# Kernel optimization log

Hardware: AMD Instinct MI355X
Metric: run time of the kernel (lower is better)

## Reference

```python
import jax, jax.numpy as jnp
import numpy as np
from jax import lax

G = 8  # number of RBF grid points (FastKAN default style)
GRID = jnp.linspace(-2.0, 2.0, G)
DENOM = 4.0 / (G - 1)  # grid spacing used as gaussian width


def _fastkan_conv(x, ln_w, ln_b, Wb, bb, Ws):
    # x: [B, C, H, W]; 3x3 conv, stride 1, pad 1 via patch unfold + FastKAN linear
    B, C, H, W = x.shape
    p = lax.conv_general_dilated_patches(x, (3, 3), (1, 1), ((1, 1), (1, 1)))  # [B, C*9, H, W]
    p = p.transpose(0, 2, 3, 1).reshape(B * H * W, C * 9)  # [N, in]
    # LayerNorm over patch features (FastKAN normalizes before the RBF basis)
    mu = p.mean(-1, keepdims=True)
    var = p.var(-1, keepdims=True)
    pn = (p - mu) / jnp.sqrt(var + 1e-5) * ln_w + ln_b
    # Gaussian RBF basis: [N, in, G]
    rbf = jnp.exp(-jnp.square((pn[:, :, None] - GRID) / DENOM))
    spline = rbf.reshape(B * H * W, -1) @ Ws.T          # [N, out]
    base = jax.nn.silu(p) @ Wb.T + bb                    # [N, out]
    out = spline + base
    return out.reshape(B, H, W, -1).transpose(0, 3, 1, 2)  # [B, out, H, W]


def _bn_relu_pool(h, gamma, beta):
    # BatchNorm2d in training mode (batch stats), ReLU, MaxPool2d(2,2)
    mu = h.mean((0, 2, 3), keepdims=True)
    var = h.var((0, 2, 3), keepdims=True)
    h = (h - mu) / jnp.sqrt(var + 1e-5) * gamma[None, :, None, None] + beta[None, :, None, None]
    h = jax.nn.relu(h)
    return lax.reduce_window(h, -jnp.inf, lax.max, (1, 1, 2, 2), (1, 1, 2, 2), 'VALID')


def setup_inputs() -> dict:
    key = jax.random.key(0)
    ks = jax.random.split(key, 16)
    B, Cin, H, W = 32, 16, 64, 64
    dims = [(Cin * 9, 64), (64 * 9, 128), (128 * 9, 256)]
    inp = {"x": jax.random.normal(ks[0], (B, Cin, H, W), jnp.float32)}
    for i, (fin, fout) in enumerate(dims, 1):
        inp[f"ln_w{i}"] = jnp.ones((fin,), jnp.float32)
        inp[f"ln_b{i}"] = jnp.zeros((fin,), jnp.float32)
        inp[f"Wb{i}"] = jax.random.normal(ks[3 * i], (fout, fin), jnp.float32) * 0.05
        inp[f"bb{i}"] = jnp.zeros((fout,), jnp.float32)
        inp[f"Ws{i}"] = jax.random.normal(ks[3 * i + 1], (fout, fin * G), jnp.float32) * 0.05
        inp[f"g{i}"] = jnp.ones((fout,), jnp.float32)
        inp[f"be{i}"] = jnp.zeros((fout,), jnp.float32)
    return inp


def reference(x, ln_w1, ln_b1, Wb1, bb1, Ws1, g1, be1,
              ln_w2, ln_b2, Wb2, bb2, Ws2, g2, be2,
              ln_w3, ln_b3, Wb3, bb3, Ws3, g3, be3):
    h = _bn_relu_pool(_fastkan_conv(x, ln_w1, ln_b1, Wb1, bb1, Ws1), g1, be1)
    h = _bn_relu_pool(_fastkan_conv(h, ln_w2, ln_b2, Wb2, bb2, Ws2), g2, be2)
    h = _bn_relu_pool(_fastkan_conv(h, ln_w3, ln_b3, Wb3, bb3, Ws3), g3, be3)
    return h.reshape(h.shape[0], -1)  # flatten: [B, 256*8*8]
```

## Files before the change

kernel.cpp:

```cpp
#include <hip/hip_runtime.h>

typedef _Float16 half_t;
typedef __attribute__((ext_vector_type(8))) _Float16 half8;
typedef __attribute__((ext_vector_type(4))) float floatx4;


#define RBF_SCALE 2.1019644f

template<int C, int H, int W>
__global__ __launch_bounds__(256)
void ln_prep(const float* __restrict__ x,
             const float* __restrict__ lnw, const float* __restrict__ lnb,
             half_t* __restrict__ pn, half_t* __restrict__ sp)
{
    const int HW = H * W, IN = C * 9;
    const int NL = (IN + 63) / 64;
    const int wv = threadIdx.x >> 6, lane = threadIdx.x & 63;
    const int pix = blockIdx.x * 4 + wv;
    const int b = pix / HW, hw = pix % HW, h = hw / W, w = hw % W;
    const float* xb = x + (long)b * C * HW;

    float v[NL];
    float s = 0.f, s2 = 0.f;
    #pragma unroll
    for (int t = 0; t < NL; ++t) {
        int i = t * 64 + lane;
        float val = 0.f;
        if (i < IN) {
            int ch = i / 9, r = i - ch * 9;
            int y = h + r / 3 - 1, xx = w + r % 3 - 1;
            if (y >= 0 && y < H && xx >= 0 && xx < W)
                val = xb[ch * HW + y * W + xx];
        }
        v[t] = val; s += val; s2 += val * val;
    }
    #pragma unroll
    for (int off = 32; off > 0; off >>= 1) {
        s  += __shfl_down(s,  off, 64);
        s2 += __shfl_down(s2, off, 64);
    }
    s = __shfl(s, 0, 64); s2 = __shfl(s2, 0, 64);
    float mean = s / IN;
    float istd = rsqrtf(s2 / IN - mean * mean + 1e-5f);

    #pragma unroll
    for (int t = 0; t < NL; ++t) {
        int i = t * 64 + lane;
        if (i < IN) {
            float val = v[t];
            float pnv = (val - mean) * istd * lnw[i] + lnb[i];
            pn[(long)pix * IN + i] = (half_t)(pnv * RBF_SCALE);
            sp[(long)pix * IN + i] = (half_t)(val / (1.f + __expf(-val)));
        }
    }
}

template<int IN, int OUT, int KPAD>
__global__ __launch_bounds__(256)
void conv_w(const float* __restrict__ Ws, const float* __restrict__ Wb,
            half_t* __restrict__ Wt)
{
    int idx = blockIdx.x * 256 + threadIdx.x;
    if (idx >= OUT * KPAD) return;
    int o = idx / KPAD, k = idx - o * KPAD;
    float v = 0.f;
    if (k < IN * 9) {
        int j = k / IN, i = k - j * IN;
        v = (j < 8) ? Ws[(long)o * IN * 8 + i * 8 + j] : Wb[(long)o * IN + i];
    }
    Wt[idx] = (half_t)v;
}

template<int IN, int OUT, int HW, int NB, int SPLIT>
__global__ __launch_bounds__(256)
void kan_gemm(const half_t* __restrict__ pn, const half_t* __restrict__ sp,
              const half_t* __restrict__ Wt, float* __restrict__ out)
{
    const int K = IN * 9, KPAD = (K + 63) & ~63, KIT = KPAD / 64;

    __shared__ half_t As[64 * 64];
    __shared__ half_t Bs[NB * 64 * 64];

    const int tid = threadIdx.x;
    const int row = tid >> 2, q = tid & 3;
    const int pix = blockIdx.x * 64 + row;
    const half_t* pnrow = pn + (long)pix * IN;
    const half_t* sprow = sp + (long)pix * IN;
    const int yoff = blockIdx.y * NB * 64;
    const half_t* wbase = Wt + (long)(yoff + row) * KPAD + q * 16;

    const int wv = tid >> 6, lane = tid & 63;
    const int lr = lane & 15, lq = lane >> 4;
    const int u0 = (2 * q) ^ (row & 7);
    const int u1 = (2 * q + 1) ^ (row & 7);

    floatx4 acc[NB][4] = {};

    const int it0 = (blockIdx.z * KIT) / SPLIT;
    const int it1 = ((blockIdx.z + 1) * KIT) / SPLIT;

    for (int it = it0; it < it1; ++it) {
        const int k0 = it * 64;
        __syncthreads();

        #pragma unroll
        for (int nb = 0; nb < NB; ++nb) {
            const uint4* src = (const uint4*)(wbase + (long)nb * 64 * KPAD + k0);
            int r2 = nb * 64 + row;
            *(uint4*)&Bs[r2 * 64 + u0 * 8] = src[0];
            *(uint4*)&Bs[r2 * 64 + u1 * 8] = src[1];
        }

        {
            int cs = k0 + q * 16;
            int j = cs / IN;
            half8 a0, a1;
            if (j < 8) {
                int i0 = cs - j * IN;
                float gj = RBF_SCALE * (-2.f + j * (4.f / 7.f));
                half8 p0 = *(const half8*)(pnrow + i0);
                half8 p1 = *(const half8*)(pnrow + i0 + 8);
                #pragma unroll
                for (int kk = 0; kk < 8; ++kk) {
                    float v0 = (float)p0[kk] - gj;
                    a0[kk] = (half_t)__builtin_amdgcn_exp2f(-(v0 * v0));
                    float v1 = (float)p1[kk] - gj;
                    a1[kk] = (half_t)__builtin_amdgcn_exp2f(-(v1 * v1));
                }
            } else if (j == 8) {
                int i0 = cs - 8 * IN;
                a0 = *(const half8*)(sprow + i0);
                a1 = *(const half8*)(sprow + i0 + 8);
            } else {
                a0 = half8{}; a1 = half8{};
            }
            *(half8*)&As[row * 64 + u0 * 8] = a0;
            *(half8*)&As[row * 64 + u1 * 8] = a1;
        }
        __syncthreads();

        #pragma unroll
        for (int ks = 0; ks < 2; ++ks) {
            half8 af[4], bf[NB];
            #pragma unroll
            for (int mf = 0; mf < 4; ++mf) {
                int r = mf * 16 + lr;
                af[mf] = *(const half8*)&As[r * 64 + (((ks * 4 + lq) ^ (r & 7)) * 8)];
            }
            #pragma unroll
            for (int nb = 0; nb < NB; ++nb) {
                int r = wv * NB * 16 + nb * 16 + lr;
                bf[nb] = *(const half8*)&Bs[r * 64 + (((ks * 4 + lq) ^ (r & 7)) * 8)];
            }
            #pragma unroll
            for (int nb = 0; nb < NB; ++nb)
                #pragma unroll
                for (int mf = 0; mf < 4; ++mf)
                    acc[nb][mf] = __builtin_amdgcn_mfma_f32_16x16x32_f16(
                        bf[nb], af[mf], acc[nb][mf], 0, 0, 0);
        }
    }

    #pragma unroll
    for (int nb = 0; nb < NB; ++nb)
    #pragma unroll
    for (int mf = 0; mf < 4; ++mf)
    #pragma unroll
    for (int reg = 0; reg < 4; ++reg) {
        int o  = yoff + wv * NB * 16 + nb * 16 + lq * 4 + reg;
        int p2 = blockIdx.x * 64 + mf * 16 + lr;
        int b2 = p2 / HW, hw2 = p2 % HW;
        long off = ((long)b2 * OUT + o) * HW + hw2;
        if (SPLIT == 1) out[off] = acc[nb][mf][reg];
        else            atomicAdd(&out[off], acc[nb][mf][reg]);
    }
}

__launch_bounds__(256)
__global__ void bn_stats(const float* __restrict__ h, const float* __restrict__ bias,
                         int C, int HW, int B, float* __restrict__ sums)
{
    int c = blockIdx.y;
    float bbc = bias[c];
    int total = B * HW;
    float s = 0.f, s2 = 0.f;
    for (int idx = blockIdx.x * 256 + threadIdx.x; idx < total; idx += 256 * gridDim.x) {
        int b = idx / HW, r = idx % HW;
        float v = h[((long)b * C + c) * HW + r] + bbc;
        s += v; s2 += v * v;
    }
    for (int off = 32; off > 0; off >>= 1) {
        s  += __shfl_down(s,  off, 64);
        s2 += __shfl_down(s2, off, 64);
    }
    __shared__ float rs[4], rs2[4];
    int lane = threadIdx.x & 63, wid = threadIdx.x >> 6;
    if (lane == 0) { rs[wid] = s; rs2[wid] = s2; }
    __syncthreads();
    if (threadIdx.x == 0) {
        atomicAdd(&sums[c],     rs[0] + rs[1] + rs[2] + rs[3]);
        atomicAdd(&sums[C + c], rs2[0] + rs2[1] + rs2[2] + rs2[3]);
    }
}

__launch_bounds__(256)
__global__ void bn_relu_pool(const float* __restrict__ h, const float* __restrict__ sums,
                             const float* __restrict__ bias,
                             const float* __restrict__ gamma, const float* __restrict__ beta,
                             float* __restrict__ out, int B, int C, int H, int W)
{
    int Ho = H / 2, Wo = W / 2;
    long total = (long)B * C * Ho * Wo;
    long idx = (long)blockIdx.x * 256 + threadIdx.x;
    if (idx >= total) return;
    int pw = idx % Wo; long t = idx / Wo;
    int ph = t % Ho; t /= Ho;
    int c = t % C; int b = (int)(t / C);

    float M = (float)B * H * W;
    float mean = sums[c] / M;
    float var  = sums[C + c] / M - mean * mean;
    float scale = gamma[c] * rsqrtf(var + 1e-5f);
    float shift = beta[c] - mean * scale + bias[c] * scale;

    const float* hp = h + ((long)b * C + c) * H * W;
    float m = 0.f;
    #pragma unroll
    for (int i = 0; i < 2; ++i)
        #pragma unroll
        for (int j = 0; j < 2; ++j) {
            float v = hp[(2 * ph + i) * W + 2 * pw + j] * scale + shift;
            m = fmaxf(m, v);
        }
    out[idx] = m;
}

extern "C" void kernel_launch(void* const* d_in, const int* in_sizes, int n_in,
                              void* d_out, int out_size, void* d_ws, size_t ws_size,
                              hipStream_t stream) {
    const float* x     = (const float*)d_in[0];
    const float* ln_w1 = (const float*)d_in[1];  const float* ln_b1 = (const float*)d_in[2];
    const float* Wb1   = (const float*)d_in[3];  const float* bb1   = (const float*)d_in[4];
    const float* Ws1   = (const float*)d_in[5];  const float* g1    = (const float*)d_in[6];
    const float* be1   = (const float*)d_in[7];
    const float* ln_w2 = (const float*)d_in[8];  const float* ln_b2 = (const float*)d_in[9];
    const float* Wb2   = (const float*)d_in[10]; const float* bb2   = (const float*)d_in[11];
    const float* Ws2   = (const float*)d_in[12]; const float* g2    = (const float*)d_in[13];
    const float* be2   = (const float*)d_in[14];
    const float* ln_w3 = (const float*)d_in[15]; const float* ln_b3 = (const float*)d_in[16];
    const float* Wb3   = (const float*)d_in[17]; const float* bb3   = (const float*)d_in[18];
    const float* Ws3   = (const float*)d_in[19]; const float* g3    = (const float*)d_in[20];
    const float* be3   = (const float*)d_in[21];

    const int B = 32;
    char* ws = (char*)d_ws;
    float*  convbuf = (float*)(ws + 0);
    float*  poolbuf = (float*)(ws + 33554432);
    float*  stats1  = (float*)(ws + 41943040);
    float*  stats2  = (float*)(ws + 41945088);
    float*  stats3  = (float*)(ws + 41947136);
    half_t* wt1     = (half_t*)(ws + 41949184);
    half_t* wt2     = (half_t*)(ws + 42121216);
    half_t* wt3     = (half_t*)(ws + 43448320);
    half_t* pnbuf   = (half_t*)(ws + 48756736);
    half_t* spbuf   = (half_t*)(ws + 86505472);

    hipMemsetAsync(stats1, 0, 6144, stream);

    conv_w<144, 64, 1344><<<(64 * 1344 + 255) / 256, 256, 0, stream>>>(Ws1, Wb1, wt1);
    conv_w<576, 128, 5184><<<(128 * 5184 + 255) / 256, 256, 0, stream>>>(Ws2, Wb2, wt2);
    conv_w<1152, 256, 10368><<<(256 * 10368 + 255) / 256, 256, 0, stream>>>(Ws3, Wb3, wt3);

    {
        const int H = 64, W = 64, OUT = 64;
        int npix = B * H * W;
        ln_prep<16, H, W><<<npix / 4, 256, 0, stream>>>(x, ln_w1, ln_b1, pnbuf, spbuf);
        kan_gemm<144, OUT, H * W, 1, 1><<<dim3(npix / 64, 1, 1), 256, 0, stream>>>(
            pnbuf, spbuf, wt1, convbuf);
        bn_stats<<<dim3(64, OUT), 256, 0, stream>>>(convbuf, bb1, OUT, H * W, B, stats1);
        long tot = (long)B * OUT * (H / 2) * (W / 2);
        bn_relu_pool<<<(tot + 255) / 256, 256, 0, stream>>>(
            convbuf, stats1, bb1, g1, be1, poolbuf, B, OUT, H, W);
    }
    {
        const int H = 32, W = 32, OUT = 128;
        int npix = B * H * W;
        ln_prep<64, H, W><<<npix / 4, 256, 0, stream>>>(poolbuf, ln_w2, ln_b2, pnbuf, spbuf);
        hipMemsetAsync(convbuf, 0, (long)npix * OUT * 4, stream);
        kan_gemm<576, OUT, H * W, 2, 2><<<dim3(npix / 64, 1, 2), 256, 0, stream>>>(
            pnbuf, spbuf, wt2, convbuf);
        bn_stats<<<dim3(16, OUT), 256, 0, stream>>>(convbuf, bb2, OUT, H * W, B, stats2);
        long tot = (long)B * OUT * (H / 2) * (W / 2);
        bn_relu_pool<<<(tot + 255) / 256, 256, 0, stream>>>(
            convbuf, stats2, bb2, g2, be2, poolbuf, B, OUT, H, W);
    }
    {
        const int H = 16, W = 16, OUT = 256;
        int npix = B * H * W;
        ln_prep<128, H, W><<<npix / 4, 256, 0, stream>>>(poolbuf, ln_w3, ln_b3, pnbuf, spbuf);
        hipMemsetAsync(convbuf, 0, (long)npix * OUT * 4, stream);
        kan_gemm<1152, OUT, H * W, 4, 6><<<dim3(npix / 64, 1, 6), 256, 0, stream>>>(
            pnbuf, spbuf, wt3, convbuf);
        bn_stats<<<dim3(8, OUT), 256, 0, stream>>>(convbuf, bb3, OUT, H * W, B, stats3);
        long tot = (long)B * OUT * (H / 2) * (W / 2);
        bn_relu_pool<<<(tot + 255) / 256, 256, 0, stream>>>(
            convbuf, stats3, bb3, g3, be3, (float*)d_out, B, OUT, H, W);
    }
}
```

Measured before the change: 548.3 us.

## Register-prefetch next K-tile in KAN GEMM and retune split-K/N tiling

The GEMM main loop now issues global loads for the next K iteration's weight tile and pn/sp inputs into registers before doing the LDS stores and MFMAs for the current tile. This hides global load latency behind compute. Layers 2 and 3 also change split-K count and N-blocking (layer 3 moves from NB=4,SPLIT=6 to NB=2 with two y-blocks and SPLIT=4), which changes grid shape and atomic traffic. The cost is extra register pressure from the prefetch buffers, which can lower occupancy.

Measured after the change: 1.191 ms. 117% more time.

```diff
diff --git a/kernel.cpp b/kernel.cpp
--- a/kernel.cpp
+++ b/kernel.cpp
@@ -99,27 +99,57 @@
     const int it0 = (blockIdx.z * KIT) / SPLIT;
     const int it1 = ((blockIdx.z + 1) * KIT) / SPLIT;
 
-    for (int it = it0; it < it1; ++it) {
+    uint4 breg[2 * NB]; half8 p0, p1; int jc;
+
+    auto issue = [&](int it, uint4* br, half8& q0, half8& q1) -> int {
         const int k0 = it * 64;
-        __syncthreads();
-
         #pragma unroll
         for (int nb = 0; nb < NB; ++nb) {
             const uint4* src = (const uint4*)(wbase + (long)nb * 64 * KPAD + k0);
+            br[2 * nb]     = src[0];
+            br[2 * nb + 1] = src[1];
+        }
+        int cs = k0 + q * 16;
+        int j = cs / IN;
+        int i0 = cs - j * IN;
+        if (j < 8) {
+            q0 = *(const half8*)(pnrow + i0);
+            q1 = *(const half8*)(pnrow + i0 + 8);
+        } else if (j == 8) {
+            q0 = *(const half8*)(sprow + i0);
+            q1 = *(const half8*)(sprow + i0 + 8);
+        } else {
+            q0 = half8{}; q1 = half8{};
+        }
+        return j;
+    };
+
+    jc = issue(it0, breg, p0, p1);
+
+    for (int it = it0; it < it1; ++it) {
+        __syncthreads();
+
+        uint4 bnx[2 * NB]; half8 n0, n1; int jn;
+        if (it + 1 < it1) {
+            jn = issue(it + 1, bnx, n0, n1);
+        } else {
+            jn = jc;
+            #pragma unroll
+            for (int t = 0; t < 2 * NB; ++t) bnx[t] = breg[t];
+            n0 = p0; n1 = p1;
+        }
+
+        #pragma unroll
+        for (int nb = 0; nb < NB; ++nb) {
             int r2 = nb * 64 + row;
-            *(uint4*)&Bs[r2 * 64 + u0 * 8] = src[0];
-            *(uint4*)&Bs[r2 * 64 + u1 * 8] = src[1];
+            *(uint4*)&Bs[r2 * 64 + u0 * 8] = breg[2 * nb];
+            *(uint4*)&Bs[r2 * 64 + u1 * 8] = breg[2 * nb + 1];
         }
 
         {
-            int cs = k0 + q * 16;
-            int j = cs / IN;
             half8 a0, a1;
-            if (j < 8) {
-                int i0 = cs - j * IN;
-                float gj = RBF_SCALE * (-2.f + j * (4.f / 7.f));
-                half8 p0 = *(const half8*)(pnrow + i0);
-                half8 p1 = *(const half8*)(pnrow + i0 + 8);
+            if (jc < 8) {
+                float gj = RBF_SCALE * (-2.f + jc * (4.f / 7.f));
                 #pragma unroll
                 for (int kk = 0; kk < 8; ++kk) {
                     float v0 = (float)p0[kk] - gj;
@@ -127,12 +157,8 @@
                     float v1 = (float)p1[kk] - gj;
                     a1[kk] = (half_t)__builtin_amdgcn_exp2f(-(v1 * v1));
                 }
-            } else if (j == 8) {
-                int i0 = cs - 8 * IN;
-                a0 = *(const half8*)(sprow + i0);
-                a1 = *(const half8*)(sprow + i0 + 8);
             } else {
-                a0 = half8{}; a1 = half8{};
+                a0 = p0; a1 = p1;
             }
             *(half8*)&As[row * 64 + u0 * 8] = a0;
             *(half8*)&As[row * 64 + u1 * 8] = a1;
@@ -159,6 +185,10 @@
                     acc[nb][mf] = __builtin_amdgcn_mfma_f32_16x16x32_f16(
                         bf[nb], af[mf], acc[nb][mf], 0, 0, 0);
         }
+
+        #pragma unroll
+        for (int t = 0; t < 2 * NB; ++t) breg[t] = bnx[t];
+        p0 = n0; p1 = n1; jc = jn;
     }
 
     #pragma unroll
@@ -287,7 +317,7 @@
         int npix = B * H * W;
         ln_prep<64, H, W><<<npix / 4, 256, 0, stream>>>(poolbuf, ln_w2, ln_b2, pnbuf, spbuf);
         hipMemsetAsync(convbuf, 0, (long)npix * OUT * 4, stream);
-        kan_gemm<576, OUT, H * W, 2, 2><<<dim3(npix / 64, 1, 2), 256, 0, stream>>>(
+        kan_gemm<576, OUT, H * W, 2, 4><<<dim3(npix / 64, 1, 4), 256, 0, stream>>>(
             pnbuf, spbuf, wt2, convbuf);
         bn_stats<<<dim3(16, OUT), 256, 0, stream>>>(convbuf, bb2, OUT, H * W, B, stats2);
         long tot = (long)B * OUT * (H / 2) * (W / 2);
@@ -299,7 +329,7 @@
         int npix = B * H * W;
         ln_prep<128, H, W><<<npix / 4, 256, 0, stream>>>(poolbuf, ln_w3, ln_b3, pnbuf, spbuf);
         hipMemsetAsync(convbuf, 0, (long)npix * OUT * 4, stream);
-        kan_gemm<1152, OUT, H * W, 4, 6><<<dim3(npix / 64, 1, 6), 256, 0, stream>>>(
+        kan_gemm<1152, OUT, H * W, 2, 4><<<dim3(npix / 64, 2, 4), 256, 0, stream>>>(
             pnbuf, spbuf, wt3, convbuf);
         bn_stats<<<dim3(8, OUT), 256, 0, stream>>>(convbuf, bb3, OUT, H * W, B, stats3);
         long tot = (long)B * OUT * (H / 2) * (W / 2);
```
